# Optimization experiments

Hardware: AMD Instinct MI355X
Metric: run time of the kernel (lower is better)

Reference implementation:

```python
import jax, jax.numpy as jnp
import numpy as np

B, S, N, D = 8, 2048, 4096, 256
MAX_W = 16  # fixed cap on span width (torch code derives it from data; padding is masked)
TINY = 1e-13  # allennlp util.masked_mean clamp


def setup_inputs() -> dict:
    key = jax.random.key(0)
    k1, k2, k3 = jax.random.split(key, 3)
    sequence_tensor = jax.random.normal(k1, (B, S, D), dtype=jnp.float32)
    starts = jax.random.randint(k2, (B, N, 1), 0, S - MAX_W)
    widths = jax.random.randint(k3, (B, N, 1), 0, MAX_W)  # width in [0, MAX_W-1]
    span_indices = jnp.concatenate([starts, starts + widths], axis=-1)  # [B,N,2], ends >= starts
    return {"sequence_tensor": sequence_tensor, "span_indices": span_indices}


def reference(sequence_tensor, span_indices):
    starts = span_indices[..., 0:1]            # [B,N,1]
    ends = span_indices[..., 1:2]              # [B,N,1]
    widths = ends - starts                     # [B,N,1]
    rng = jnp.arange(MAX_W)[None, None, :]     # [1,1,W]
    raw_idx = ends - rng                       # [B,N,W] indices counting back from end
    span_mask = ((rng <= widths) & (raw_idx >= 0)).astype(sequence_tensor.dtype)  # [B,N,W]
    idx = jnp.maximum(raw_idx, 0)              # relu(raw).long()
    batch_ids = jnp.arange(sequence_tensor.shape[0])[:, None, None]
    span_embeddings = sequence_tensor[batch_ids, idx]  # gather -> [B,N,W,D]
    summed = jnp.einsum('bnwd,bnw->bnd', span_embeddings, span_mask)
    count = jnp.maximum(jnp.sum(span_mask, axis=-1, keepdims=True), TINY)  # [B,N,1]
    return summed / count  # masked mean over span positions -> [B,N,D]
```

## Files before the change

kernel.cpp:

```cpp
#include <hip/hip_runtime.h>
#include <hip/hip_bf16.h>

#define PB 8
#define PS 2048
#define PN 4096
#define PD 256

__global__ __launch_bounds__(256) void span_mean_kernel(
    const float* __restrict__ seq,
    const int*   __restrict__ spans,
    float*       __restrict__ out)
{
    const int span = (blockIdx.x << 2) | (threadIdx.x >> 6);
    const int lane = threadIdx.x & 63;

    const int b = span >> 12;

    const int2 se    = ((const int2*)spans)[span];
    const int  start = se.x;
    const int  width = se.y - se.x;

    const float inv = 1.0f / (float)(width + 1);

    const float* base = seq + (((size_t)b * PS + (size_t)start) * PD) + (lane << 2);

    float4 acc = make_float4(0.f, 0.f, 0.f, 0.f);
    for (int w = 0; w <= width; ++w) {
        const float4 v = *(const float4*)(base + (size_t)w * PD);
        acc.x += v.x; acc.y += v.y; acc.z += v.z; acc.w += v.w;
    }
    acc.x *= inv; acc.y *= inv; acc.z *= inv; acc.w *= inv;

    *(float4*)(out + (size_t)span * PD + (lane << 2)) = acc;
}

extern "C" void kernel_launch(void* const* d_in, const int* in_sizes, int n_in,
                              void* d_out, int out_size, void* d_ws, size_t ws_size,
                              hipStream_t stream) {
    const float* seq   = (const float*)d_in[0];
    const int*   spans = (const int*)d_in[1];
    float*       out   = (float*)d_out;

    const int n_spans = PB * PN;
    dim3 grid(n_spans / 4);
    dim3 block(256);
    span_mean_kernel<<<grid, block, 0, stream>>>(seq, spans, out);
}
```

Measured before the change: 93.45 us.

## Replace per-span row summation with prefix-sum differences over sequence

Span means are now computed from a prefix sum of the sequence along the position axis. One pass sums fixed-size chunks, a small kernel scans the chunk totals, a third pass writes the full exclusive prefix array into workspace, and a final gather takes the difference of two prefix rows per span and divides by the count. This replaces the variable-length loop over up to 16 rows per span with exactly two row loads. In exchange it adds three extra kernel launches and a full read and write of a sequence-sized workspace, and the prefix passes use only a few hundred blocks. Subtracting large running sums can also lose floating-point precision.

Measured after the change: 87.95 us. -5.9%, faster.

```diff
diff --git a/kernel.cpp b/kernel.cpp
--- a/kernel.cpp
+++ b/kernel.cpp
@@ -5,33 +5,78 @@
 #define PS 2048
 #define PN 4096
 #define PD 256
+#define CHUNK 64
+#define NCHUNK (PS / CHUNK)
 
-__global__ __launch_bounds__(256) void span_mean_kernel(
-    const float* __restrict__ seq,
-    const int*   __restrict__ spans,
-    float*       __restrict__ out)
-{
-    const int span = (blockIdx.x << 2) | (threadIdx.x >> 6);
-    const int lane = threadIdx.x & 63;
+__global__ __launch_bounds__(256) void k_chunksum(const float* __restrict__ seq,
+                                                  float* __restrict__ csum) {
+    const int b = blockIdx.x & 7;
+    const int c = blockIdx.x >> 3;
+    const int d = threadIdx.x;
+    const float* p = seq + (((size_t)b * PS + (size_t)c * CHUNK) * PD) + d;
+    float s = 0.f;
+    #pragma unroll 16
+    for (int i = 0; i < CHUNK; ++i) s += p[(size_t)i * PD];
+    csum[((size_t)b * NCHUNK + c) * PD + d] = s;
+}
 
-    const int b = span >> 12;
+__global__ __launch_bounds__(256) void k_chunkscan(const float* __restrict__ csum,
+                                                   float* __restrict__ coff) {
+    const int b = blockIdx.x;
+    const int d = threadIdx.x;
+    float v[NCHUNK];
+    #pragma unroll
+    for (int c = 0; c < NCHUNK; ++c)
+        v[c] = csum[((size_t)b * NCHUNK + c) * PD + d];
+    float run = 0.f;
+    #pragma unroll
+    for (int c = 0; c < NCHUNK; ++c) {
+        coff[((size_t)b * NCHUNK + c) * PD + d] = run;
+        run += v[c];
+    }
+}
 
-    const int2 se    = ((const int2*)spans)[span];
-    const int  start = se.x;
-    const int  width = se.y - se.x;
+__global__ __launch_bounds__(256) void k_writeP(const float* __restrict__ seq,
+                                                const float* __restrict__ coff,
+                                                float* __restrict__ P) {
+    const int b = blockIdx.x & 7;
+    const int c = blockIdx.x >> 3;
+    const int d = threadIdx.x;
+    const size_t rowbase = ((size_t)b * PS + (size_t)c * CHUNK) * PD + d;
+    const float* ps = seq + rowbase;
+    float*       pp = P   + rowbase;
+    float run = coff[((size_t)b * NCHUNK + c) * PD + d];
+    #pragma unroll 8
+    for (int i = 0; i < CHUNK; ++i) {
+        const float x = ps[(size_t)i * PD];
+        pp[(size_t)i * PD] = run;
+        run += x;
+    }
+}
 
-    const float inv = 1.0f / (float)(width + 1);
+__global__ __launch_bounds__(256) void k_gather(const float* __restrict__ P,
+                                               const int*   __restrict__ spans,
+                                               float*       __restrict__ out) {
+    const int b       = blockIdx.x & 7;
+    const int blk     = blockIdx.x >> 3;
+    const int span_ib = (blk << 2) | (threadIdx.x >> 6);
+    const int span    = (b << 12) | span_ib;
+    const int lane    = threadIdx.x & 63;
 
-    const float* base = seq + (((size_t)b * PS + (size_t)start) * PD) + (lane << 2);
+    const int2 se = ((const int2*)spans)[span];
+    const float inv = 1.0f / (float)(se.y - se.x + 1);
 
-    float4 acc = make_float4(0.f, 0.f, 0.f, 0.f);
-    for (int w = 0; w <= width; ++w) {
-        const float4 v = *(const float4*)(base + (size_t)w * PD);
-        acc.x += v.x; acc.y += v.y; acc.z += v.z; acc.w += v.w;
-    }
-    acc.x *= inv; acc.y *= inv; acc.z *= inv; acc.w *= inv;
+    const float* Pb = P + ((size_t)b * PS) * PD + (lane << 2);
+    const float4 p0 = *(const float4*)(Pb + (size_t)se.x       * PD);
+    const float4 p1 = *(const float4*)(Pb + (size_t)(se.y + 1) * PD);
 
-    *(float4*)(out + (size_t)span * PD + (lane << 2)) = acc;
+    float4 r;
+    r.x = (p1.x - p0.x) * inv;
+    r.y = (p1.y - p0.y) * inv;
+    r.z = (p1.z - p0.z) * inv;
+    r.w = (p1.w - p0.w) * inv;
+
+    *(float4*)(out + (size_t)span * PD + (lane << 2)) = r;
 }
 
 extern "C" void kernel_launch(void* const* d_in, const int* in_sizes, int n_in,
@@ -41,8 +86,12 @@
     const int*   spans = (const int*)d_in[1];
     float*       out   = (float*)d_out;
 
-    const int n_spans = PB * PN;
-    dim3 grid(n_spans / 4);
-    dim3 block(256);
-    span_mean_kernel<<<grid, block, 0, stream>>>(seq, spans, out);
+    float* P    = (float*)d_ws;
+    float* csum = P    + (size_t)PB * PS * PD;
+    float* coff = csum + (size_t)PB * NCHUNK * PD;
+
+    k_chunksum <<<dim3(PB * NCHUNK), dim3(256), 0, stream>>>(seq, csum);
+    k_chunkscan<<<dim3(PB),          dim3(256), 0, stream>>>(csum, coff);
+    k_writeP   <<<dim3(PB * NCHUNK), dim3(256), 0, stream>>>(seq, coff, P);
+    k_gather   <<<dim3(PB * PN / 4), dim3(256), 0, stream>>>(P, spans, out);
 }
```

## Issue all span row loads up front, interleave batches across blocks

Applied to the files above, without the earlier changes.

Replaces the serial accumulation loop with a fall-through switch that issues every row load for the span before any add, then sums them into four independent accumulators. The goal is more loads in flight per wave, so memory latency is hidden instead of exposed once per row. Start and width go through readfirstlane so they are scalar, and the output is written with nontemporal stores. Block indexing now interleaves the batch across consecutive blocks, which changes the locality pattern. The cost is higher register pressure from up to sixteen live vector loads, and the code assumes width never exceeds 15.

New measurement: 86.85 us. 7.1% less time.

```diff
diff --git a/kernel.cpp b/kernel.cpp
--- a/kernel.cpp
+++ b/kernel.cpp
@@ -6,32 +6,73 @@
 #define PN 4096
 #define PD 256
 
+typedef float vf4 __attribute__((ext_vector_type(4)));
+
 __global__ __launch_bounds__(256) void span_mean_kernel(
     const float* __restrict__ seq,
     const int*   __restrict__ spans,
     float*       __restrict__ out)
 {
-    const int span = (blockIdx.x << 2) | (threadIdx.x >> 6);
-    const int lane = threadIdx.x & 63;
-
-    const int b = span >> 12;
+    const int b       = blockIdx.x & 7;
+    const int blk     = blockIdx.x >> 3;
+    const int span_ib = (blk << 2) | (threadIdx.x >> 6);
+    const int span    = (b << 12) | span_ib;
+    const int lane    = threadIdx.x & 63;
 
     const int2 se    = ((const int2*)spans)[span];
-    const int  start = se.x;
-    const int  width = se.y - se.x;
+    const int  start = __builtin_amdgcn_readfirstlane(se.x);
+    const int  width = __builtin_amdgcn_readfirstlane(se.y) - start;
 
     const float inv = 1.0f / (float)(width + 1);
 
-    const float* base = seq + (((size_t)b * PS + (size_t)start) * PD) + (lane << 2);
+    const float* base = seq + (((size_t)b * PS + start) * PD) + (lane << 2);
+#define LD(w) (*(const vf4*)(base + (w) * PD))
 
-    float4 acc = make_float4(0.f, 0.f, 0.f, 0.f);
-    for (int w = 0; w <= width; ++w) {
-        const float4 v = *(const float4*)(base + (size_t)w * PD);
-        acc.x += v.x; acc.y += v.y; acc.z += v.z; acc.w += v.w;
+    vf4 A = LD(0);
+
+    vf4 v1, v2, v3, v4, v5, v6, v7, v8, v9, v10, v11, v12, v13, v14, v15;
+    switch (width) {
+        case 15: v15 = LD(15); [[fallthrough]];
+        case 14: v14 = LD(14); [[fallthrough]];
+        case 13: v13 = LD(13); [[fallthrough]];
+        case 12: v12 = LD(12); [[fallthrough]];
+        case 11: v11 = LD(11); [[fallthrough]];
+        case 10: v10 = LD(10); [[fallthrough]];
+        case 9:  v9  = LD(9);  [[fallthrough]];
+        case 8:  v8  = LD(8);  [[fallthrough]];
+        case 7:  v7  = LD(7);  [[fallthrough]];
+        case 6:  v6  = LD(6);  [[fallthrough]];
+        case 5:  v5  = LD(5);  [[fallthrough]];
+        case 4:  v4  = LD(4);  [[fallthrough]];
+        case 3:  v3  = LD(3);  [[fallthrough]];
+        case 2:  v2  = LD(2);  [[fallthrough]];
+        case 1:  v1  = LD(1);  break;
+        default: break;
     }
-    acc.x *= inv; acc.y *= inv; acc.z *= inv; acc.w *= inv;
 
-    *(float4*)(out + (size_t)span * PD + (lane << 2)) = acc;
+    vf4 Bq = {0.f, 0.f, 0.f, 0.f};
+    vf4 Cq = {0.f, 0.f, 0.f, 0.f};
+    vf4 Dq = {0.f, 0.f, 0.f, 0.f};
+    if (width >= 1)  Bq += v1;
+    if (width >= 2)  Cq += v2;
+    if (width >= 3)  Dq += v3;
+    if (width >= 4)  A  += v4;
+    if (width >= 5)  Bq += v5;
+    if (width >= 6)  Cq += v6;
+    if (width >= 7)  Dq += v7;
+    if (width >= 8)  A  += v8;
+    if (width >= 9)  Bq += v9;
+    if (width >= 10) Cq += v10;
+    if (width >= 11) Dq += v11;
+    if (width >= 12) A  += v12;
+    if (width >= 13) Bq += v13;
+    if (width >= 14) Cq += v14;
+    if (width >= 15) Dq += v15;
+
+    vf4 r = ((A + Bq) + (Cq + Dq)) * inv;
+
+    __builtin_nontemporal_store(r, (vf4*)(out + (size_t)span * PD + (lane << 2)));
+#undef LD
 }
 
 extern "C" void kernel_launch(void* const* d_in, const int* in_sizes, int n_in,
```

## Replace per-span summation with chunked prefix/suffix sums and two-lookup gather

Applied to the files above, without the earlier changes.

Adds a pre-pass that, for each 16-row chunk of the sequence, writes inclusive prefix sums (Q) and suffix sums (R) into workspace. Each span mean then needs at most two row reads instead of up to 16, because spans never exceed 16 rows and so cross at most one chunk boundary. The pre-pass adds a full read of the sequence and writes two sequence-sized buffers plus an extra launch, and the prefix/suffix arithmetic can shift float rounding slightly. The gather also uses readfirstlane for the span bounds, batch-interleaved block ordering, and nontemporal output stores.

Result: faster. 87.92 us (-5.9%).

```diff
diff --git a/kernel.cpp b/kernel.cpp
--- a/kernel.cpp
+++ b/kernel.cpp
@@ -5,33 +5,61 @@
 #define PS 2048
 #define PN 4096
 #define PD 256
+#define RCH 16
+#define NRCH (PS / RCH)
 
-__global__ __launch_bounds__(256) void span_mean_kernel(
-    const float* __restrict__ seq,
-    const int*   __restrict__ spans,
-    float*       __restrict__ out)
-{
-    const int span = (blockIdx.x << 2) | (threadIdx.x >> 6);
-    const int lane = threadIdx.x & 63;
+typedef float vf4 __attribute__((ext_vector_type(4)));
 
-    const int b = span >> 12;
+__global__ __launch_bounds__(256) void k_buildQR(const float* __restrict__ seq,
+                                                 float* __restrict__ Q,
+                                                 float* __restrict__ R) {
+    const int b = blockIdx.x & 7;
+    const int c = blockIdx.x >> 3;
+    const int d = threadIdx.x;
+    const size_t base = ((size_t)b * PS + (size_t)c * RCH) * PD + d;
 
-    const int2 se    = ((const int2*)spans)[span];
-    const int  start = se.x;
-    const int  width = se.y - se.x;
+    float x[RCH];
+    #pragma unroll
+    for (int i = 0; i < RCH; ++i) x[i] = seq[base + (size_t)i * PD];
 
-    const float inv = 1.0f / (float)(width + 1);
+    float q = 0.f;
+    #pragma unroll
+    for (int i = 0; i < RCH; ++i) { q += x[i]; Q[base + (size_t)i * PD] = q; }
 
-    const float* base = seq + (((size_t)b * PS + (size_t)start) * PD) + (lane << 2);
+    float r = 0.f;
+    #pragma unroll
+    for (int i = RCH - 1; i >= 0; --i) { r += x[i]; R[base + (size_t)i * PD] = r; }
+}
 
-    float4 acc = make_float4(0.f, 0.f, 0.f, 0.f);
-    for (int w = 0; w <= width; ++w) {
-        const float4 v = *(const float4*)(base + (size_t)w * PD);
-        acc.x += v.x; acc.y += v.y; acc.z += v.z; acc.w += v.w;
+__global__ __launch_bounds__(256) void k_gather(const float* __restrict__ Q,
+                                               const float* __restrict__ R,
+                                               const int*   __restrict__ spans,
+                                               float*       __restrict__ out) {
+    const int b       = blockIdx.x & 7;
+    const int blk     = blockIdx.x >> 3;
+    const int span_ib = (blk << 2) | (threadIdx.x >> 6);
+    const int span    = (b << 12) | span_ib;
+    const int lane    = threadIdx.x & 63;
+
+    const int2 se   = ((const int2*)spans)[span];
+    const int start = __builtin_amdgcn_readfirstlane(se.x);
+    const int end   = __builtin_amdgcn_readfirstlane(se.y);
+    const float inv = 1.0f / (float)(end - start + 1);
+
+    const size_t rowoff = (size_t)b * PS * PD + (lane << 2);
+
+    const vf4 a = *(const vf4*)(Q + rowoff + (size_t)end * PD);
+    vf4 s;
+    if ((start >> 4) != (end >> 4)) {
+        s = a + *(const vf4*)(R + rowoff + (size_t)start * PD);
+    } else if (start & 15) {
+        s = a - *(const vf4*)(Q + rowoff + (size_t)(start - 1) * PD);
+    } else {
+        s = a;
     }
-    acc.x *= inv; acc.y *= inv; acc.z *= inv; acc.w *= inv;
+    const vf4 r = s * inv;
 
-    *(float4*)(out + (size_t)span * PD + (lane << 2)) = acc;
+    __builtin_nontemporal_store(r, (vf4*)(out + (size_t)span * PD + (lane << 2)));
 }
 
 extern "C" void kernel_launch(void* const* d_in, const int* in_sizes, int n_in,
@@ -41,8 +69,9 @@
     const int*   spans = (const int*)d_in[1];
     float*       out   = (float*)d_out;
 
-    const int n_spans = PB * PN;
-    dim3 grid(n_spans / 4);
-    dim3 block(256);
-    span_mean_kernel<<<grid, block, 0, stream>>>(seq, spans, out);
+    float* Q = (float*)d_ws;
+    float* R = Q + (size_t)PB * PS * PD;
+
+    k_buildQR<<<dim3(PB * NRCH),   dim3(256), 0, stream>>>(seq, Q, R);
+    k_gather <<<dim3(PB * PN / 4), dim3(256), 0, stream>>>(Q, R, spans, out);
 }
```
